# Optimization experiments

Hardware: AMD Instinct MI355X
Metric: run time of the kernel (lower is better)

## Reference

```python
import jax, jax.numpy as jnp
import numpy as np

EPS = 1e-06
NUM_HEADS = 8


def phi(x):
    # elu(x) + 1, a positive feature map
    return jax.nn.elu(x) + 1.0


def setup_inputs() -> dict:
    key = jax.random.key(0)
    ks = jax.random.split(key, 7)
    B, N, E = 4, 1024, 512
    s = 1.0 / np.sqrt(E)
    return {
        "Q": jax.random.normal(ks[0], (B, N, E), jnp.float32),
        "K": jax.random.normal(ks[1], (B, N, E), jnp.float32),
        "V": jax.random.normal(ks[2], (B, N, E), jnp.float32),
        "Wq": jax.random.normal(ks[3], (E, E), jnp.float32) * s,
        "Wk": jax.random.normal(ks[4], (E, E), jnp.float32) * s,
        "Wv": jax.random.normal(ks[5], (E, E), jnp.float32) * s,
        "Wo": jax.random.normal(ks[6], (E, E), jnp.float32) * s,
        "causal": 1,
    }


def _split_heads(x, H):
    B, N, E = x.shape
    return x.reshape(B, N, H, E // H).transpose(0, 2, 1, 3)  # (B,H,N,D)


def reference(Q, K, V, Wq, Wk, Wv, Wo, causal):
    B, N, E = Q.shape
    H = NUM_HEADS
    D = E // H
    # nn.Linear: y = x @ W.T (bias=False)
    Qf = phi(_split_heads(Q @ Wq.T, H))  # (B,H,N,D)
    Kf = phi(_split_heads(K @ Wk.T, H))  # (B,H,N,D)
    Vh = _split_heads(V @ Wv.T, H)       # (B,H,N,D)

    if causal:
        # prefix sums of outer products K_f V^T -> (B,H,N,D,Dv)
        KV_prefix = jnp.cumsum(Kf[..., :, None] * Vh[..., None, :], axis=2)
        Kf_prefix = jnp.cumsum(Kf, axis=2)
        num = jnp.einsum('bhnd,bhnde->bhne', Qf, KV_prefix)
        den = jnp.einsum('bhnd,bhnd->bhn', Qf, Kf_prefix)[..., None]
        out = num / (den + EPS)
    else:
        KV = jnp.einsum('bhnd,bhne->bhde', Kf, Vh)          # (B,H,D,Dv)
        Kf_sum = Kf.sum(axis=2)                              # (B,H,D)
        num = jnp.einsum('bhnd,bhde->bhne', Qf, KV)
        den = jnp.einsum('bhnd,bhd->bhn', Qf, Kf_sum)[..., None]
        out = num / (den + EPS)

    out = out.transpose(0, 2, 1, 3).reshape(B, N, E)
    return out @ Wo.T
```

## Files before the change

### kernel.cpp

```cpp
#include <hip/hip_runtime.h>
#include <stdint.h>

typedef __bf16 bf16;
typedef __attribute__((ext_vector_type(8))) __bf16 bfx8;
typedef __attribute__((ext_vector_type(4))) float f32x4;

__device__ inline f32x4 mfma16(bfx8 a, bfx8 b, f32x4 c) {
  return __builtin_amdgcn_mfma_f32_16x16x32_bf16(a, b, c, 0, 0, 0);
}

__device__ inline void gl16(const bf16* g, bf16* lbase, int lane) {
#if __has_builtin(__builtin_amdgcn_global_load_lds)
  (void)lane;
  __builtin_amdgcn_global_load_lds(
      (const __attribute__((address_space(1))) void*)g,
      (__attribute__((address_space(3))) void*)lbase, 16, 0, 0);
#else
  *(bfx8*)(lbase + lane * 8) = *(const bfx8*)g;
#endif
}

__device__ inline int img_off(int i, int e) {
  return i * 64 + ((((e >> 3) ^ (i & 7)) << 3)) + (e & 7);
}

struct CvtArgs {
  const float* src[4];
  bf16* dst[4];
};
__global__ __launch_bounds__(256) void cvt_w(CvtArgs ca) {
  const int z = blockIdx.y;
  const int T = blockIdx.x * 256 + threadIdx.x;
  const int n = T >> 3, s8 = T & 7, i = n & 63, nt = n >> 6;
  const float* src = ca.src[z];
  bf16* dst = ca.dst[z];
#pragma unroll
  for (int kt = 0; kt < 8; ++kt) {
    const float* s = src + (size_t)n * 512 + kt * 64 + ((s8 ^ (i & 7)) << 3);
    f32x4 x0 = *(const f32x4*)s, x1 = *(const f32x4*)(s + 4);
    bfx8 v;
    v[0] = (bf16)x0[0]; v[1] = (bf16)x0[1]; v[2] = (bf16)x0[2]; v[3] = (bf16)x0[3];
    v[4] = (bf16)x1[0]; v[5] = (bf16)x1[1]; v[6] = (bf16)x1[2]; v[7] = (bf16)x1[3];
    *(bfx8*)&dst[(size_t)(kt * 8 + nt) * 4096 + i * 64 + s8 * 8] = v;
  }
}

struct GemmArgs {
  const void* A[3];
  const bf16* Bt[3];
  bf16* ob[3];
  float* of;
  int phi_upto;
};

template <bool AF32, bool OUTF>
__global__ __launch_bounds__(256) void gemm_bt(GemmArgs ga) {
  const int z = blockIdx.z;
  const void* Ag = ga.A[z];
  const bf16* Bg = ga.Bt[z];
  const int tm = blockIdx.x * 64, by = blockIdx.y, tn = by * 128;
  const int tid = threadIdx.x, l = tid & 63, w = tid >> 6;
  const int wm = w >> 1, wn = w & 1, lm = l & 15, lk = l >> 4;

  __shared__ __align__(16) bf16 As[64 * 64];
  __shared__ __align__(16) bf16 Bs[128 * 64];

  f32x4 acc[2][4] = {};

  for (int kt = 0; kt < 8; ++kt) {
    const bf16* bsrc = Bg + (size_t)(kt * 8 + by * 2) * 4096;
#pragma unroll
    for (int q = 0; q < 4; ++q) {
      int cb = (q * 4 + w) * 64;
      gl16(bsrc + (size_t)(cb + l) * 8, &Bs[cb * 8], l);
    }
    if (AF32) {
#pragma unroll
      for (int it = 0; it < 2; ++it) {
        int c = it * 256 + tid;
        int row = c >> 3, t8 = c & 7;
        const float* s = (const float*)Ag + (size_t)(tm + row) * 512 + kt * 64 + t8 * 8;
        f32x4 x0 = *(const f32x4*)s, x1 = *(const f32x4*)(s + 4);
        bfx8 v;
        v[0] = (bf16)x0[0]; v[1] = (bf16)x0[1]; v[2] = (bf16)x0[2]; v[3] = (bf16)x0[3];
        v[4] = (bf16)x1[0]; v[5] = (bf16)x1[1]; v[6] = (bf16)x1[2]; v[7] = (bf16)x1[3];
        *(bfx8*)&As[row * 64 + ((t8 ^ (row & 7)) << 3)] = v;
      }
    } else {
      const bf16* asrc = (const bf16*)Ag + ((size_t)((tm >> 6) * 8 + kt) << 12);
#pragma unroll
      for (int q = 0; q < 2; ++q) {
        int cb = (q * 4 + w) * 64;
        gl16(asrc + (size_t)(cb + l) * 8, &As[cb * 8], l);
      }
    }
    __syncthreads();
#pragma unroll
    for (int ks = 0; ks < 2; ++ks) {
      bfx8 af[2], bfr[4];
#pragma unroll
      for (int i = 0; i < 2; ++i) {
        int ra = wm * 32 + i * 16 + lm;
        af[i] = *(const bfx8*)&As[ra * 64 + (((ks * 4 + lk) ^ (ra & 7)) << 3)];
      }
#pragma unroll
      for (int j = 0; j < 4; ++j) {
        int rb = wn * 64 + j * 16 + lm;
        bfr[j] = *(const bfx8*)&Bs[rb * 64 + (((ks * 4 + lk) ^ (rb & 7)) << 3)];
      }
#pragma unroll
      for (int i = 0; i < 2; ++i)
#pragma unroll
        for (int j = 0; j < 4; ++j)
          acc[i][j] = mfma16(af[i], bfr[j], acc[i][j]);
    }
    __syncthreads();
  }

  const bool phi = z < ga.phi_upto;
#pragma unroll
  for (int i = 0; i < 2; ++i)
#pragma unroll
    for (int j = 0; j < 4; ++j)
#pragma unroll
      for (int r = 0; r < 4; ++r) {
        int m = tm + wm * 32 + i * 16 + lk * 4 + r;
        int n = tn + wn * 64 + j * 16 + lm;
        float v = acc[i][j][r];
        if (phi) v = v > 0.f ? v + 1.f : __expf(v);
        if (OUTF) {
          ga.of[(size_t)m * 512 + n] = v;
        } else {
          ga.ob[z][((size_t)((m >> 6) * 8 + (n >> 6)) << 12) + img_off(m & 63, n & 63)] =
              (bf16)v;
        }
      }
}

__global__ __launch_bounds__(256) void chunk_kv(const bf16* __restrict__ Kimg,
                                                const bf16* __restrict__ Vimg,
                                                bf16* __restrict__ KVb,
                                                float* __restrict__ ksums) {
  const int bh = blockIdx.x, c = blockIdx.y, b = bh >> 3, h = bh & 7;
  const int tid = threadIdx.x, l = tid & 63, w = tid >> 6, lm = l & 15, lk = l >> 4;
  __shared__ __align__(16) bf16 KTs[64 * 64];
  __shared__ __align__(16) bf16 VTs[64 * 64];
  __shared__ float ksum_p[256];

  const size_t tb = (size_t)((b * 16 + c) * 8 + h) << 12;
  const bf16* Kt = Kimg + tb;
  const bf16* Vt = Vimg + tb;
  const int sr = tid >> 2, sp = tid & 3;
  {
    bfx8 k0 = *(const bfx8*)&Kt[sr * 64 + (((2 * sp) ^ (sr & 7)) << 3)];
    bfx8 k1 = *(const bfx8*)&Kt[sr * 64 + (((2 * sp + 1) ^ (sr & 7)) << 3)];
    bfx8 v0 = *(const bfx8*)&Vt[sr * 64 + (((2 * sp) ^ (sr & 7)) << 3)];
    bfx8 v1 = *(const bfx8*)&Vt[sr * 64 + (((2 * sp + 1) ^ (sr & 7)) << 3)];
#pragma unroll
    for (int q = 0; q < 8; ++q) {
      int d0 = sp * 16 + q, d1 = sp * 16 + 8 + q;
      KTs[d0 * 64 + (((sr >> 3) ^ (d0 & 7)) << 3) + (sr & 7)] = k0[q];
      KTs[d1 * 64 + (((sr >> 3) ^ (d1 & 7)) << 3) + (sr & 7)] = k1[q];
      VTs[d0 * 64 + (((sr >> 3) ^ (d0 & 7)) << 3) + (sr & 7)] = v0[q];
      VTs[d1 * 64 + (((sr >> 3) ^ (d1 & 7)) << 3) + (sr & 7)] = v1[q];
    }
  }
  __syncthreads();
  {
    int d = tid & 63, jp = tid >> 6;
    float s = 0.f;
#pragma unroll
    for (int q = 0; q < 16; ++q) {
      int j = jp * 16 + q;
      s += (float)KTs[d * 64 + (((j >> 3) ^ (d & 7)) << 3) + (j & 7)];
    }
    ksum_p[jp * 64 + d] = s;
  }
  f32x4 kacc[4] = {};
#pragma unroll
  for (int ks = 0; ks < 2; ++ks) {
    int r = w * 16 + lm;
    bfx8 av = *(const bfx8*)&VTs[r * 64 + (((ks * 4 + lk) ^ (r & 7)) << 3)];
#pragma unroll
    for (int bn = 0; bn < 4; ++bn) {
      int e = bn * 16 + lm;
      bfx8 bk = *(const bfx8*)&KTs[e * 64 + (((ks * 4 + lk) ^ (e & 7)) << 3)];
      kacc[bn] = mfma16(av, bk, kacc[bn]);
    }
  }
  bf16* st = KVb + (size_t)(bh * 16 + c) * 4096;
#pragma unroll
  for (int bn = 0; bn < 4; ++bn)
#pragma unroll
    for (int rg = 0; rg < 4; ++rg) {
      int e = w * 16 + lk * 4 + rg, d = bn * 16 + lm;
      st[e * 64 + d] = (bf16)kacc[bn][rg];
    }
  __syncthreads();
  if (tid < 64)
    ksums[(size_t)(bh * 16 + c) * 64 + tid] =
        ksum_p[tid] + ksum_p[64 + tid] + ksum_p[128 + tid] + ksum_p[192 + tid];
}

__global__ __launch_bounds__(256) void chunk_out(const bf16* __restrict__ Qimg,
                                                 const bf16* __restrict__ Kimg,
                                                 const bf16* __restrict__ Vimg,
                                                 const bf16* __restrict__ KVb,
                                                 const float* __restrict__ ksums,
                                                 bf16* __restrict__ Obsw) {
  const int bh = blockIdx.x, c = blockIdx.y, b = bh >> 3, h = bh & 7;
  const int tid = threadIdx.x, l = tid & 63, w = tid >> 6, lm = l & 15, lk = l >> 4;

  __shared__ __align__(16) bf16 Qs[64 * 64];
  __shared__ __align__(16) bf16 Ks[64 * 64];
  __shared__ __align__(16) bf16 VTs[64 * 64];
  __shared__ __align__(16) bf16 Ss[64 * 64];
  __shared__ __align__(16) bf16 KVL[64 * 64];
  __shared__ float ksum[64], den_i[64], den_all[64], den_p[256];

  const size_t tb = (size_t)((b * 16 + c) * 8 + h) << 12;
  const int sr = tid >> 2, sp = tid & 3;

#pragma unroll
  for (int q = 0; q < 2; ++q) {
    int cb = (q * 4 + w) * 64;
    gl16(Qimg + tb + (size_t)(cb + l) * 8, &Qs[cb * 8], l);
    gl16(Kimg + tb + (size_t)(cb + l) * 8, &Ks[cb * 8], l);
  }
  {
    const bf16* Vt = Vimg + tb;
    bfx8 v0 = *(const bfx8*)&Vt[sr * 64 + (((2 * sp) ^ (sr & 7)) << 3)];
    bfx8 v1 = *(const bfx8*)&Vt[sr * 64 + (((2 * sp + 1) ^ (sr & 7)) << 3)];
#pragma unroll
    for (int q = 0; q < 8; ++q) {
      int d0 = sp * 16 + q, d1 = sp * 16 + 8 + q;
      VTs[d0 * 64 + (((sr >> 3) ^ (d0 & 7)) << 3) + (sr & 7)] = v0[q];
      VTs[d1 * 64 + (((sr >> 3) ^ (d1 & 7)) << 3) + (sr & 7)] = v1[q];
    }
  }
  {
    const int e = sr, dp = sp * 16;
    float s0[8] = {}, s1[8] = {};
    const bf16* kb = KVb + (size_t)(bh * 16) * 4096 + e * 64 + dp;
    for (int cc = 0; cc < c; ++cc) {
      bfx8 x0 = *(const bfx8*)(kb + (size_t)cc * 4096);
      bfx8 x1 = *(const bfx8*)(kb + (size_t)cc * 4096 + 8);
#pragma unroll
      for (int q = 0; q < 8; ++q) { s0[q] += (float)x0[q]; s1[q] += (float)x1[q]; }
    }
    bfx8 y0, y1;
#pragma unroll
    for (int q = 0; q < 8; ++q) { y0[q] = (bf16)s0[q]; y1[q] = (bf16)s1[q]; }
    *(bfx8*)&KVL[e * 64 + (((2 * sp) ^ (e & 7)) << 3)] = y0;
    *(bfx8*)&KVL[e * 64 + (((2 * sp + 1) ^ (e & 7)) << 3)] = y1;
    if (tid < 64) {
      float s = 0.f;
      const float* kp = ksums + (size_t)(bh * 16) * 64 + tid;
      for (int cc = 0; cc < c; ++cc) s += kp[(size_t)cc * 64];
      ksum[tid] = s;
    }
  }
  __syncthreads();

  f32x4 sacc[4] = {};
  bfx8 aq[2];
#pragma unroll
  for (int ks = 0; ks < 2; ++ks) {
    int r = w * 16 + lm;
    aq[ks] = *(const bfx8*)&Qs[r * 64 + (((ks * 4 + lk) ^ (r & 7)) << 3)];
#pragma unroll
    for (int bn = 0; bn < 4; ++bn) {
// ... 31 lines not shown
    den_p[sp * 64 + sr] = s;
  }
  __syncthreads();

  if (tid < 64)
    den_all[tid] = den_i[tid] + den_p[tid] + den_p[64 + tid] + den_p[128 + tid] + den_p[192 + tid];
  f32x4 oacc[4] = {};
#pragma unroll
  for (int ks = 0; ks < 2; ++ks) {
    int r = w * 16 + lm;
    bfx8 as_ = *(const bfx8*)&Ss[r * 64 + (((ks * 4 + lk) ^ (r & 7)) << 3)];
#pragma unroll
    for (int bn = 0; bn < 4; ++bn) {
      int e = bn * 16 + lm;
      bfx8 bv = *(const bfx8*)&VTs[e * 64 + (((ks * 4 + lk) ^ (e & 7)) << 3)];
      oacc[bn] = mfma16(as_, bv, oacc[bn]);
      bfx8 bkv = *(const bfx8*)&KVL[e * 64 + (((ks * 4 + lk) ^ (e & 7)) << 3)];
      oacc[bn] = mfma16(aq[ks], bkv, oacc[bn]);
    }
  }
  __syncthreads();

  bf16* ot = Obsw + tb;
#pragma unroll
  for (int bn = 0; bn < 4; ++bn)
#pragma unroll
    for (int rg = 0; rg < 4; ++rg) {
      int i = w * 16 + lk * 4 + rg, e = bn * 16 + lm;
      float o = oacc[bn][rg] / (den_all[i] + 1e-6f);
      ot[img_off(i, e)] = (bf16)o;
    }
}

extern "C" void kernel_launch(void* const* d_in, const int* in_sizes, int n_in,
                              void* d_out, int out_size, void* d_ws, size_t ws_size,
                              hipStream_t stream) {
  const float* Q = (const float*)d_in[0];
  const float* K = (const float*)d_in[1];
  const float* V = (const float*)d_in[2];
  const float* Wq = (const float*)d_in[3];
  const float* Wk = (const float*)d_in[4];
  const float* Wv = (const float*)d_in[5];
  const float* Wo = (const float*)d_in[6];
  (void)in_sizes; (void)n_in; (void)out_size; (void)ws_size;

  char* wsp = (char*)d_ws;
  const size_t MB = 1ull << 20;
  const size_t HK = 512 * 1024;
  bf16* Wimg[4];
  for (int z = 0; z < 4; ++z) Wimg[z] = (bf16*)(wsp + z * HK);
  bf16* Qimg = (bf16*)(wsp + 4 * MB);
  bf16* Kimg = (bf16*)(wsp + 8 * MB);
  bf16* Vimg = (bf16*)(wsp + 12 * MB);
  bf16* Obsw = (bf16*)(wsp + 16 * MB);
  bf16* KVb = (bf16*)(wsp + 20 * MB);
  float* ksums = (float*)(wsp + 24 * MB);

  CvtArgs ca;
  ca.src[0] = Wq; ca.src[1] = Wk; ca.src[2] = Wv; ca.src[3] = Wo;
  ca.dst[0] = Wimg[0]; ca.dst[1] = Wimg[1]; ca.dst[2] = Wimg[2]; ca.dst[3] = Wimg[3];
  cvt_w<<<dim3(16, 4), 256, 0, stream>>>(ca);

  GemmArgs g1;
  g1.A[0] = Q;  g1.A[1] = K;  g1.A[2] = V;
  g1.Bt[0] = Wimg[0]; g1.Bt[1] = Wimg[1]; g1.Bt[2] = Wimg[2];
  g1.ob[0] = Qimg; g1.ob[1] = Kimg; g1.ob[2] = Vimg;
  g1.of = nullptr;
  g1.phi_upto = 2;
  gemm_bt<true, false><<<dim3(64, 4, 3), 256, 0, stream>>>(g1);

  chunk_kv<<<dim3(32, 16), 256, 0, stream>>>(Kimg, Vimg, KVb, ksums);
  chunk_out<<<dim3(32, 16), 256, 0, stream>>>(Qimg, Kimg, Vimg, KVb, ksums, Obsw);

  GemmArgs g2;
  g2.A[0] = Obsw; g2.A[1] = nullptr; g2.A[2] = nullptr;
  g2.Bt[0] = Wimg[3]; g2.Bt[1] = nullptr; g2.Bt[2] = nullptr;
  g2.ob[0] = nullptr; g2.ob[1] = nullptr; g2.ob[2] = nullptr;
  g2.of = (float*)d_out;
  g2.phi_upto = 0;
  gemm_bt<false, true><<<dim3(64, 4, 1), 256, 0, stream>>>(g2);
}
```

Baseline: 48.30 us.

## Double-buffer GEMM tiles and reuse transposed V image from chunk_kv in chunk_out

The GEMM kernel now double-buffers its A and B shared tiles, prefetching the next k-tile (DMA for B and bf16 A, register staging for fp32 A) while computing the current one, and drops one barrier per iteration. chunk_kv now loads K/V tiles into LDS via global_load_lds before transposing, and writes the transposed V tile to a new workspace image. chunk_out then DMA-loads that pre-transposed V instead of redoing the scalar LDS transpose. The cost is doubled GEMM LDS (lower occupancy), extra registers, and an extra global write and buffer for V^T.

```diff
diff --git a/kernel.cpp b/kernel.cpp
--- a/kernel.cpp
+++ b/kernel.cpp
@@ -62,51 +62,79 @@
   const int tid = threadIdx.x, l = tid & 63, w = tid >> 6;
   const int wm = w >> 1, wn = w & 1, lm = l & 15, lk = l >> 4;
 
-  __shared__ __align__(16) bf16 As[64 * 64];
-  __shared__ __align__(16) bf16 Bs[128 * 64];
+  __shared__ __align__(16) bf16 As[2][64 * 64];
+  __shared__ __align__(16) bf16 Bs[2][128 * 64];
 
   f32x4 acc[2][4] = {};
-
-  for (int kt = 0; kt < 8; ++kt) {
+  f32x4 a_reg[2][2];
+
+  auto issueB = [&](int kt, int buf) {
     const bf16* bsrc = Bg + (size_t)(kt * 8 + by * 2) * 4096;
 #pragma unroll
     for (int q = 0; q < 4; ++q) {
       int cb = (q * 4 + w) * 64;
-      gl16(bsrc + (size_t)(cb + l) * 8, &Bs[cb * 8], l);
-    }
-    if (AF32) {
-#pragma unroll
-      for (int it = 0; it < 2; ++it) {
-        int c = it * 256 + tid;
-        int row = c >> 3, t8 = c & 7;
-        const float* s = (const float*)Ag + (size_t)(tm + row) * 512 + kt * 64 + t8 * 8;
-        f32x4 x0 = *(const f32x4*)s, x1 = *(const f32x4*)(s + 4);
-        bfx8 v;
-        v[0] = (bf16)x0[0]; v[1] = (bf16)x0[1]; v[2] = (bf16)x0[2]; v[3] = (bf16)x0[3];
-        v[4] = (bf16)x1[0]; v[5] = (bf16)x1[1]; v[6] = (bf16)x1[2]; v[7] = (bf16)x1[3];
-        *(bfx8*)&As[row * 64 + ((t8 ^ (row & 7)) << 3)] = v;
-      }
-    } else {
-      const bf16* asrc = (const bf16*)Ag + ((size_t)((tm >> 6) * 8 + kt) << 12);
-#pragma unroll
-      for (int q = 0; q < 2; ++q) {
-        int cb = (q * 4 + w) * 64;
-        gl16(asrc + (size_t)(cb + l) * 8, &As[cb * 8], l);
-      }
-    }
-    __syncthreads();
+      gl16(bsrc + (size_t)(cb + l) * 8, &Bs[buf][cb * 8], l);
+    }
+  };
+  auto issueA_dma = [&](int kt, int buf) {
+    const bf16* asrc = (const bf16*)Ag + ((size_t)((tm >> 6) * 8 + kt) << 12);
+#pragma unroll
+    for (int q = 0; q < 2; ++q) {
+      int cb = (q * 4 + w) * 64;
+      gl16(asrc + (size_t)(cb + l) * 8, &As[buf][cb * 8], l);
+    }
+  };
+  auto loadA = [&](int kt) {
+#pragma unroll
+    for (int it = 0; it < 2; ++it) {
+      int c = it * 256 + tid;
+      int row = c >> 3, t8 = c & 7;
+      const float* s = (const float*)Ag + (size_t)(tm + row) * 512 + kt * 64 + t8 * 8;
+      a_reg[it][0] = *(const f32x4*)s;
+      a_reg[it][1] = *(const f32x4*)(s + 4);
+    }
+  };
+  auto writeA = [&](int buf) {
+#pragma unroll
+    for (int it = 0; it < 2; ++it) {
+      int c = it * 256 + tid;
+      int row = c >> 3, t8 = c & 7;
+      bfx8 v;
+      f32x4 x0 = a_reg[it][0], x1 = a_reg[it][1];
+      v[0] = (bf16)x0[0]; v[1] = (bf16)x0[1]; v[2] = (bf16)x0[2]; v[3] = (bf16)x0[3];
+      v[4] = (bf16)x1[0]; v[5] = (bf16)x1[1]; v[6] = (bf16)x1[2]; v[7] = (bf16)x1[3];
+      *(bfx8*)&As[buf][row * 64 + ((t8 ^ (row & 7)) << 3)] = v;
+    }
+  };
+
+  issueB(0, 0);
+  if constexpr (AF32) {
+    loadA(0);
+    writeA(0);
+  } else {
+    issueA_dma(0, 0);
+  }
+  __syncthreads();
+
+  for (int kt = 0; kt < 8; ++kt) {
+    const int cur = kt & 1, nxt = cur ^ 1;
+    if (kt < 7) {
+      issueB(kt + 1, nxt);
+      if constexpr (AF32) loadA(kt + 1);
+      else issueA_dma(kt + 1, nxt);
+    }
 #pragma unroll
     for (int ks = 0; ks < 2; ++ks) {
       bfx8 af[2], bfr[4];
 #pragma unroll
       for (int i = 0; i < 2; ++i) {
         int ra = wm * 32 + i * 16 + lm;
-        af[i] = *(const bfx8*)&As[ra * 64 + (((ks * 4 + lk) ^ (ra & 7)) << 3)];
+        af[i] = *(const bfx8*)&As[cur][ra * 64 + (((ks * 4 + lk) ^ (ra & 7)) << 3)];
       }
 #pragma unroll
       for (int j = 0; j < 4; ++j) {
         int rb = wn * 64 + j * 16 + lm;
-        bfr[j] = *(const bfx8*)&Bs[rb * 64 + (((ks * 4 + lk) ^ (rb & 7)) << 3)];
+        bfr[j] = *(const bfx8*)&Bs[cur][rb * 64 + (((ks * 4 + lk) ^ (rb & 7)) << 3)];
       }
 #pragma unroll
       for (int i = 0; i < 2; ++i)
@@ -114,7 +142,10 @@
         for (int j = 0; j < 4; ++j)
           acc[i][j] = mfma16(af[i], bfr[j], acc[i][j]);
     }
-    __syncthreads();
+    if (kt < 7) {
+      if constexpr (AF32) writeA(nxt);
+      __syncthreads();
+    }
   }
 
   const bool phi = z < ga.phi_upto;
@@ -140,22 +171,32 @@
 __global__ __launch_bounds__(256) void chunk_kv(const bf16* __restrict__ Kimg,
                                                 const bf16* __restrict__ Vimg,
                                                 bf16* __restrict__ KVb,
-                                                float* __restrict__ ksums) {
+                                                float* __restrict__ ksums,
+                                                bf16* __restrict__ VTimg) {
   const int bh = blockIdx.x, c = blockIdx.y, b = bh >> 3, h = bh & 7;
   const int tid = threadIdx.x, l = tid & 63, w = tid >> 6, lm = l & 15, lk = l >> 4;
+  __shared__ __align__(16) bf16 Ks[64 * 64];
+  __shared__ __align__(16) bf16 Vs[64 * 64];
   __shared__ __align__(16) bf16 KTs[64 * 64];
   __shared__ __align__(16) bf16 VTs[64 * 64];
   __shared__ float ksum_p[256];
 
   const size_t tb = (size_t)((b * 16 + c) * 8 + h) << 12;
-  const bf16* Kt = Kimg + tb;
-  const bf16* Vt = Vimg + tb;
   const int sr = tid >> 2, sp = tid & 3;
+
+#pragma unroll
+  for (int q = 0; q < 2; ++q) {
+    int cb = (q * 4 + w) * 64;
+    gl16(Kimg + tb + (size_t)(cb + l) * 8, &Ks[cb * 8], l);
+    gl16(Vimg + tb + (size_t)(cb + l) * 8, &Vs[cb * 8], l);
+  }
+  __syncthreads();
+
   {
-    bfx8 k0 = *(const bfx8*)&Kt[sr * 64 + (((2 * sp) ^ (sr & 7)) << 3)];
-    bfx8 k1 = *(const bfx8*)&Kt[sr * 64 + (((2 * sp + 1) ^ (sr & 7)) << 3)];
-    bfx8 v0 = *(const bfx8*)&Vt[sr * 64 + (((2 * sp) ^ (sr & 7)) << 3)];
-    bfx8 v1 = *(const bfx8*)&Vt[sr * 64 + (((2 * sp + 1) ^ (sr & 7)) << 3)];
+    bfx8 k0 = *(const bfx8*)&Ks[sr * 64 + (((2 * sp) ^ (sr & 7)) << 3)];
+    bfx8 k1 = *(const bfx8*)&Ks[sr * 64 + (((2 * sp + 1) ^ (sr & 7)) << 3)];
+    bfx8 v0 = *(const bfx8*)&Vs[sr * 64 + (((2 * sp) ^ (sr & 7)) << 3)];
+    bfx8 v1 = *(const bfx8*)&Vs[sr * 64 + (((2 * sp + 1) ^ (sr & 7)) << 3)];
 #pragma unroll
     for (int q = 0; q < 8; ++q) {
       int d0 = sp * 16 + q, d1 = sp * 16 + 8 + q;
@@ -166,6 +207,7 @@
     }
   }
   __syncthreads();
+
   {
     int d = tid & 63, jp = tid >> 6;
     float s = 0.f;
@@ -175,6 +217,11 @@
       s += (float)KTs[d * 64 + (((j >> 3) ^ (d & 7)) << 3) + (j & 7)];
     }
     ksum_p[jp * 64 + d] = s;
+  }
+#pragma unroll
+  for (int q = 0; q < 2; ++q) {
+    int cid = q * 256 + tid;
+    *(bfx8*)&VTimg[tb + (size_t)cid * 8] = *(const bfx8*)&VTs[cid * 8];
   }
   f32x4 kacc[4] = {};
 #pragma unroll
@@ -204,7 +251,7 @@
 
 __global__ __launch_bounds__(256) void chunk_out(const bf16* __restrict__ Qimg,
                                                  const bf16* __restrict__ Kimg,
-                                                 const bf16* __restrict__ Vimg,
+                                                 const bf16* __restrict__ VTimg,
                                                  const bf16* __restrict__ KVb,
                                                  const float* __restrict__ ksums,
                                                  bf16* __restrict__ Obsw) {
@@ -226,17 +273,7 @@
     int cb = (q * 4 + w) * 64;
     gl16(Qimg + tb + (size_t)(cb + l) * 8, &Qs[cb * 8], l);
     gl16(Kimg + tb + (size_t)(cb + l) * 8, &Ks[cb * 8], l);
-  }
-  {
-    const bf16* Vt = Vimg + tb;
-    bfx8 v0 = *(const bfx8*)&Vt[sr * 64 + (((2 * sp) ^ (sr & 7)) << 3)];
-    bfx8 v1 = *(const bfx8*)&Vt[sr * 64 + (((2 * sp + 1) ^ (sr & 7)) << 3)];
-#pragma unroll
-    for (int q = 0; q < 8; ++q) {
-      int d0 = sp * 16 + q, d1 = sp * 16 + 8 + q;
-      VTs[d0 * 64 + (((sr >> 3) ^ (d0 & 7)) << 3) + (sr & 7)] = v0[q];
-      VTs[d1 * 64 + (((sr >> 3) ^ (d1 & 7)) << 3) + (sr & 7)] = v1[q];
-    }
+    gl16(VTimg + tb + (size_t)(cb + l) * 8, &VTs[cb * 8], l);
   }
   {
     const int e = sr, dp = sp * 16;
@@ -357,6 +394,7 @@
   bf16* Obsw = (bf16*)(wsp + 16 * MB);
   bf16* KVb = (bf16*)(wsp + 20 * MB);
   float* ksums = (float*)(wsp + 24 * MB);
+  bf16* VTimg = (bf16*)(wsp + 28 * MB);
 
   CvtArgs ca;
   ca.src[0] = Wq; ca.src[1] = Wk; ca.src[2] = Wv; ca.src[3] = Wo;
@@ -371,8 +409,8 @@
   g1.phi_upto = 2;
   gemm_bt<true, false><<<dim3(64, 4, 3), 256, 0, stream>>>(g1);
 
-  chunk_kv<<<dim3(32, 16), 256, 0, stream>>>(Kimg, Vimg, KVb, ksums);
-  chunk_out<<<dim3(32, 16), 256, 0, stream>>>(Qimg, Kimg, Vimg, KVb, ksums, Obsw);
+  chunk_kv<<<dim3(32, 16), 256, 0, stream>>>(Kimg, Vimg, KVb, ksums, VTimg);
+  chunk_out<<<dim3(32, 16), 256, 0, stream>>>(Qimg, Kimg, VTimg, KVb, ksums, Obsw);
 
   GemmArgs g2;
   g2.A[0] = Obsw; g2.A[1] = nullptr; g2.A[2] = nullptr;
```

After: 49.35 us. +2.2%, slower.

## Fuse weight conversion, QKV projections and chunk KV into fewer kernels

Applied to the files above, without the earlier changes.

Removes the separate weight-conversion kernel by converting fp32 weights to bf16 on the fly inside each GEMM's tile load. Merges the K and V projections with the per-chunk KV outer-product and key-sum computation in one block, keeping K and V tiles in shared memory instead of re-reading them from global memory. This cuts the launch count from five to three. In exchange every block reconverts weight tiles redundantly, and K/V blocks run two serial GEMMs, so those blocks carry much more work than the Q blocks and the load becomes unbalanced.

```diff
diff --git a/kernel.cpp b/kernel.cpp
--- a/kernel.cpp
+++ b/kernel.cpp
@@ -24,75 +24,110 @@
   return i * 64 + ((((e >> 3) ^ (i & 7)) << 3)) + (e & 7);
 }
 
-struct CvtArgs {
-  const float* src[4];
-  bf16* dst[4];
+__device__ inline bfx8 cvt8(const float* s) {
+  f32x4 x0 = *(const f32x4*)s, x1 = *(const f32x4*)(s + 4);
+  bfx8 v;
+  v[0] = (bf16)x0[0]; v[1] = (bf16)x0[1]; v[2] = (bf16)x0[2]; v[3] = (bf16)x0[3];
+  v[4] = (bf16)x1[0]; v[5] = (bf16)x1[1]; v[6] = (bf16)x1[2]; v[7] = (bf16)x1[3];
+  return v;
+}
+
+struct ProjArgs {
+  const float *Q, *K, *V, *Wq, *Wk, *Wv;
+  bf16 *Qimg, *Kimg, *Vimg, *KVb;
+  float* ksums;
 };
-__global__ __launch_bounds__(256) void cvt_w(CvtArgs ca) {
-  const int z = blockIdx.y;
-  const int T = blockIdx.x * 256 + threadIdx.x;
-  const int n = T >> 3, s8 = T & 7, i = n & 63, nt = n >> 6;
-  const float* src = ca.src[z];
-  bf16* dst = ca.dst[z];
-#pragma unroll
-  for (int kt = 0; kt < 8; ++kt) {
-    const float* s = src + (size_t)n * 512 + kt * 64 + ((s8 ^ (i & 7)) << 3);
-    f32x4 x0 = *(const f32x4*)s, x1 = *(const f32x4*)(s + 4);
-    bfx8 v;
-    v[0] = (bf16)x0[0]; v[1] = (bf16)x0[1]; v[2] = (bf16)x0[2]; v[3] = (bf16)x0[3];
-    v[4] = (bf16)x1[0]; v[5] = (bf16)x1[1]; v[6] = (bf16)x1[2]; v[7] = (bf16)x1[3];
-    *(bfx8*)&dst[(size_t)(kt * 8 + nt) * 4096 + i * 64 + s8 * 8] = v;
-  }
-}
-
-struct GemmArgs {
-  const void* A[3];
-  const bf16* Bt[3];
-  bf16* ob[3];
-  float* of;
-  int phi_upto;
-};
-
-template <bool AF32, bool OUTF>
-__global__ __launch_bounds__(256) void gemm_bt(GemmArgs ga) {
-  const int z = blockIdx.z;
-  const void* Ag = ga.A[z];
-  const bf16* Bg = ga.Bt[z];
-  const int tm = blockIdx.x * 64, by = blockIdx.y, tn = by * 128;
+
+__global__ __launch_bounds__(256) void proj_fused(ProjArgs pa) {
   const int tid = threadIdx.x, l = tid & 63, w = tid >> 6;
   const int wm = w >> 1, wn = w & 1, lm = l & 15, lk = l >> 4;
-
-  __shared__ __align__(16) bf16 As[64 * 64];
-  __shared__ __align__(16) bf16 Bs[128 * 64];
-
-  f32x4 acc[2][4] = {};
-
+  __shared__ __align__(16) char smem[41984];
+  bf16* As = (bf16*)smem;
+  bf16* Bs = (bf16*)(smem + 8192);
+
+  const int bid = blockIdx.x;
+  const int idx = bid >> 1;
+
+  if ((bid & 1) == 0) {
+    const int tm = (idx >> 2) * 64, tn = (idx & 3) * 128;
+    f32x4 acc[2][4] = {};
+    for (int kt = 0; kt < 8; ++kt) {
+#pragma unroll
+      for (int it = 0; it < 4; ++it) {
+        int c = it * 256 + tid, row = c >> 3, t8 = c & 7;
+        bfx8 v = cvt8(pa.Wq + (size_t)(tn + row) * 512 + kt * 64 + t8 * 8);
+        *(bfx8*)&Bs[row * 64 + ((t8 ^ (row & 7)) << 3)] = v;
+      }
+#pragma unroll
+      for (int it = 0; it < 2; ++it) {
+        int c = it * 256 + tid, row = c >> 3, t8 = c & 7;
+        bfx8 v = cvt8(pa.Q + (size_t)(tm + row) * 512 + kt * 64 + t8 * 8);
+        *(bfx8*)&As[row * 64 + ((t8 ^ (row & 7)) << 3)] = v;
+      }
+      __syncthreads();
+#pragma unroll
+      for (int ks = 0; ks < 2; ++ks) {
+        bfx8 af[2], bfr[4];
+#pragma unroll
+        for (int i = 0; i < 2; ++i) {
+          int ra = wm * 32 + i * 16 + lm;
+          af[i] = *(const bfx8*)&As[ra * 64 + (((ks * 4 + lk) ^ (ra & 7)) << 3)];
+        }
+#pragma unroll
+        for (int j = 0; j < 4; ++j) {
+          int rb = wn * 64 + j * 16 + lm;
+          bfr[j] = *(const bfx8*)&Bs[rb * 64 + (((ks * 4 + lk) ^ (rb & 7)) << 3)];
+        }
+#pragma unroll
+        for (int i = 0; i < 2; ++i)
+#pragma unroll
+          for (int j = 0; j < 4; ++j)
+            acc[i][j] = mfma16(af[i], bfr[j], acc[i][j]);
+      }
+      __syncthreads();
+    }
+#pragma unroll
+    for (int i = 0; i < 2; ++i)
+#pragma unroll
+      for (int j = 0; j < 4; ++j)
+#pragma unroll
+        for (int r = 0; r < 4; ++r) {
+          int m = tm + wm * 32 + i * 16 + lk * 4 + r;
+          int n = tn + wn * 64 + j * 16 + lm;
+          float v = acc[i][j][r];
+          v = v > 0.f ? v + 1.f : __expf(v);
+          pa.Qimg[((size_t)((m >> 6) * 8 + (n >> 6)) << 12) + img_off(m & 63, n & 63)] =
+              (bf16)v;
+        }
+    return;
+  }
+
+  const int rt = idx >> 2, ty = idx & 3;
+  const int tm = rt * 64, tn = ty * 128;
+  bf16* VT0 = (bf16*)smem;
+  bf16* VT1 = (bf16*)(smem + 8192);
+  bf16* KT0 = (bf16*)(smem + 24576);
+  bf16* KT1 = (bf16*)(smem + 32768);
+  float* ksum_p = (float*)(smem + 40960);
+
+  f32x4 acc[2][4];
+
+#pragma unroll
+  for (int i = 0; i < 2; ++i)
+#pragma unroll
+    for (int j = 0; j < 4; ++j) acc[i][j] = (f32x4){0.f, 0.f, 0.f, 0.f};
   for (int kt = 0; kt < 8; ++kt) {
-    const bf16* bsrc = Bg + (size_t)(kt * 8 + by * 2) * 4096;
-#pragma unroll
-    for (int q = 0; q < 4; ++q) {
-      int cb = (q * 4 + w) * 64;
-      gl16(bsrc + (size_t)(cb + l) * 8, &Bs[cb * 8], l);
-    }
-    if (AF32) {
-#pragma unroll
-      for (int it = 0; it < 2; ++it) {
-        int c = it * 256 + tid;
-        int row = c >> 3, t8 = c & 7;
-        const float* s = (const float*)Ag + (size_t)(tm + row) * 512 + kt * 64 + t8 * 8;
-        f32x4 x0 = *(const f32x4*)s, x1 = *(const f32x4*)(s + 4);
-        bfx8 v;
-        v[0] = (bf16)x0[0]; v[1] = (bf16)x0[1]; v[2] = (bf16)x0[2]; v[3] = (bf16)x0[3];
-        v[4] = (bf16)x1[0]; v[5] = (bf16)x1[1]; v[6] = (bf16)x1[2]; v[7] = (bf16)x1[3];
-        *(bfx8*)&As[row * 64 + ((t8 ^ (row & 7)) << 3)] = v;
-      }
-    } else {
-      const bf16* asrc = (const bf16*)Ag + ((size_t)((tm >> 6) * 8 + kt) << 12);
-#pragma unroll
-      for (int q = 0; q < 2; ++q) {
-        int cb = (q * 4 + w) * 64;
-        gl16(asrc + (size_t)(cb + l) * 8, &As[cb * 8], l);
-      }
+#pragma unroll
+    for (int it = 0; it < 4; ++it) {
+      int c = it * 256 + tid, row = c >> 3, t8 = c & 7;
+      bfx8 v = cvt8(pa.Wk + (size_t)(tn + row) * 512 + kt * 64 + t8 * 8);
+      *(bfx8*)&Bs[row * 64 + ((t8 ^ (row & 7)) << 3)] = v;
+    }
+#pragma unroll
+    for (int it = 0; it < 2; ++it) {
+      int c = it * 256 + tid, row = c >> 3, t8 = c & 7;
+      bfx8 v = cvt8(pa.K + (size_t)(tm + row) * 512 + kt * 64 + t8 * 8);
+      *(bfx8*)&As[row * 64 + ((t8 ^ (row & 7)) << 3)] = v;
     }
     __syncthreads();
 #pragma unroll
@@ -116,90 +151,123 @@
     }
     __syncthreads();
   }
-
-  const bool phi = z < ga.phi_upto;
+  {
+    bf16* KTl = wn ? KT1 : KT0;
+#pragma unroll
+    for (int i = 0; i < 2; ++i)
+#pragma unroll
+      for (int jj = 0; jj < 4; ++jj)
+#pragma unroll
+        for (int r = 0; r < 4; ++r) {
+          int ml = wm * 32 + i * 16 + lk * 4 + r;
+          int dl = jj * 16 + lm;
+          float v = acc[i][jj][r];
+          v = v > 0.f ? v + 1.f : __expf(v);
+          bf16 bv = (bf16)v;
+          KTl[dl * 64 + (((ml >> 3) ^ (dl & 7)) << 3) + (ml & 7)] = bv;
+          pa.Kimg[((size_t)(rt * 8 + 2 * ty + wn) << 12) + img_off(ml, dl)] = bv;
+        }
+  }
+  __syncthreads();
+
 #pragma unroll
   for (int i = 0; i < 2; ++i)
 #pragma unroll
-    for (int j = 0; j < 4; ++j)
-#pragma unroll
-      for (int r = 0; r < 4; ++r) {
-        int m = tm + wm * 32 + i * 16 + lk * 4 + r;
-        int n = tn + wn * 64 + j * 16 + lm;
-        float v = acc[i][j][r];
-        if (phi) v = v > 0.f ? v + 1.f : __expf(v);
-        if (OUTF) {
-          ga.of[(size_t)m * 512 + n] = v;
-        } else {
-          ga.ob[z][((size_t)((m >> 6) * 8 + (n >> 6)) << 12) + img_off(m & 63, n & 63)] =
-              (bf16)v;
+    for (int j = 0; j < 4; ++j) acc[i][j] = (f32x4){0.f, 0.f, 0.f, 0.f};
+  for (int kt = 0; kt < 8; ++kt) {
+#pragma unroll
+    for (int it = 0; it < 4; ++it) {
+      int c = it * 256 + tid, row = c >> 3, t8 = c & 7;
+      bfx8 v = cvt8(pa.Wv + (size_t)(tn + row) * 512 + kt * 64 + t8 * 8);
+      *(bfx8*)&Bs[row * 64 + ((t8 ^ (row & 7)) << 3)] = v;
+    }
+#pragma unroll
+    for (int it = 0; it < 2; ++it) {
+      int c = it * 256 + tid, row = c >> 3, t8 = c & 7;
+      bfx8 v = cvt8(pa.V + (size_t)(tm + row) * 512 + kt * 64 + t8 * 8);
+      *(bfx8*)&As[row * 64 + ((t8 ^ (row & 7)) << 3)] = v;
+    }
+    __syncthreads();
+#pragma unroll
+    for (int ks = 0; ks < 2; ++ks) {
+      bfx8 af[2], bfr[4];
+#pragma unroll
+      for (int i = 0; i < 2; ++i) {
+        int ra = wm * 32 + i * 16 + lm;
+        af[i] = *(const bfx8*)&As[ra * 64 + (((ks * 4 + lk) ^ (ra & 7)) << 3)];
+      }
+#pragma unroll
+      for (int j = 0; j < 4; ++j) {
+        int rb = wn * 64 + j * 16 + lm;
+        bfr[j] = *(const bfx8*)&Bs[rb * 64 + (((ks * 4 + lk) ^ (rb & 7)) << 3)];
+      }
+#pragma unroll
+      for (int i = 0; i < 2; ++i)
+#pragma unroll
+        for (int j = 0; j < 4; ++j)
+          acc[i][j] = mfma16(af[i], bfr[j], acc[i][j]);
+    }
+    __syncthreads();
+  }
+  {
+    bf16* VTl = wn ? VT1 : VT0;
+#pragma unroll
+    for (int i = 0; i < 2; ++i)
+#pragma unroll
+      for (int jj = 0; jj < 4; ++jj)
+#pragma unroll
+        for (int r = 0; r < 4; ++r) {
+          int ml = wm * 32 + i * 16 + lk * 4 + r;
+          int dl = jj * 16 + lm;
+          bf16 bv = (bf16)acc[i][jj][r];
+          VTl[dl * 64 + (((ml >> 3) ^ (dl & 7)) << 3) + (ml & 7)] = bv;
+          pa.Vimg[((size_t)(rt * 8 + 2 * ty + wn) << 12) + img_off(ml, dl)] = bv;
         }
-      }
-}
-
-__global__ __launch_bounds__(256) void chunk_kv(const bf16* __restrict__ Kimg,
-                                                const bf16* __restrict__ Vimg,
-                                                bf16* __restrict__ KVb,
-                                                float* __restrict__ ksums) {
-  const int bh = blockIdx.x, c = blockIdx.y, b = bh >> 3, h = bh & 7;
-  const int tid = threadIdx.x, l = tid & 63, w = tid >> 6, lm = l & 15, lk = l >> 4;
-  __shared__ __align__(16) bf16 KTs[64 * 64];
-  __shared__ __align__(16) bf16 VTs[64 * 64];
-  __shared__ float ksum_p[256];
-
-  const size_t tb = (size_t)((b * 16 + c) * 8 + h) << 12;
-  const bf16* Kt = Kimg + tb;
-  const bf16* Vt = Vimg + tb;
-  const int sr = tid >> 2, sp = tid & 3;
-  {
-    bfx8 k0 = *(const bfx8*)&Kt[sr * 64 + (((2 * sp) ^ (sr & 7)) << 3)];
-    bfx8 k1 = *(const bfx8*)&Kt[sr * 64 + (((2 * sp + 1) ^ (sr & 7)) << 3)];
-    bfx8 v0 = *(const bfx8*)&Vt[sr * 64 + (((2 * sp) ^ (sr & 7)) << 3)];
-    bfx8 v1 = *(const bfx8*)&Vt[sr * 64 + (((2 * sp + 1) ^ (sr & 7)) << 3)];
-#pragma unroll
-    for (int q = 0; q < 8; ++q) {
-      int d0 = sp * 16 + q, d1 = sp * 16 + 8 + q;
-      KTs[d0 * 64 + (((sr >> 3) ^ (d0 & 7)) << 3) + (sr & 7)] = k0[q];
-      KTs[d1 * 64 + (((sr >> 3) ^ (d1 & 7)) << 3) + (sr & 7)] = k1[q];
-      VTs[d0 * 64 + (((sr >> 3) ^ (d0 & 7)) << 3) + (sr & 7)] = v0[q];
-      VTs[d1 * 64 + (((sr >> 3) ^ (d1 & 7)) << 3) + (sr & 7)] = v1[q];
-    }
   }
   __syncthreads();
-  {
-    int d = tid & 63, jp = tid >> 6;
-    float s = 0.f;
-#pragma unroll
-    for (int q = 0; q < 16; ++q) {
-      int j = jp * 16 + q;
-      s += (float)KTs[d * 64 + (((j >> 3) ^ (d & 7)) << 3) + (j & 7)];
-    }
-    ksum_p[jp * 64 + d] = s;
-  }
-  f32x4 kacc[4] = {};
-#pragma unroll
-  for (int ks = 0; ks < 2; ++ks) {
-    int r = w * 16 + lm;
-    bfx8 av = *(const bfx8*)&VTs[r * 64 + (((ks * 4 + lk) ^ (r & 7)) << 3)];
-#pragma unroll
-    for (int bn = 0; bn < 4; ++bn) {
-      int e = bn * 16 + lm;
-      bfx8 bk = *(const bfx8*)&KTs[e * 64 + (((ks * 4 + lk) ^ (e & 7)) << 3)];
-      kacc[bn] = mfma16(av, bk, kacc[bn]);
-    }
-  }
-  bf16* st = KVb + (size_t)(bh * 16 + c) * 4096;
-#pragma unroll
-  for (int bn = 0; bn < 4; ++bn)
-#pragma unroll
-    for (int rg = 0; rg < 4; ++rg) {
-      int e = w * 16 + lk * 4 + rg, d = bn * 16 + lm;
-      st[e * 64 + d] = (bf16)kacc[bn][rg];
-    }
-  __syncthreads();
-  if (tid < 64)
-    ksums[(size_t)(bh * 16 + c) * 64 + tid] =
-        ksum_p[tid] + ksum_p[64 + tid] + ksum_p[128 + tid] + ksum_p[192 + tid];
+
+  const int b = rt >> 4, c = rt & 15;
+#pragma unroll
+  for (int hh = 0; hh < 2; ++hh) {
+    const bf16* KTl = hh ? KT1 : KT0;
+    const bf16* VTl = hh ? VT1 : VT0;
+    {
+      int d = tid & 63, jp = tid >> 6;
+      float s = 0.f;
+#pragma unroll
+      for (int q = 0; q < 16; ++q) {
+        int j = jp * 16 + q;
+        s += (float)KTl[d * 64 + (((j >> 3) ^ (d & 7)) << 3) + (j & 7)];
+      }
+      ksum_p[jp * 64 + d] = s;
+    }
+    f32x4 kacc[4] = {};
+#pragma unroll
+    for (int ks = 0; ks < 2; ++ks) {
+      int r = w * 16 + lm;
+      bfx8 av = *(const bfx8*)&VTl[r * 64 + (((ks * 4 + lk) ^ (r & 7)) << 3)];
+#pragma unroll
+      for (int bn = 0; bn < 4; ++bn) {
+        int e = bn * 16 + lm;
+        bfx8 bk = *(const bfx8*)&KTl[e * 64 + (((ks * 4 + lk) ^ (e & 7)) << 3)];
+        kacc[bn] = mfma16(av, bk, kacc[bn]);
+      }
+    }
+    const int bh = b * 8 + 2 * ty + hh;
+    bf16* st = pa.KVb + (size_t)(bh * 16 + c) * 4096;
+#pragma unroll
+    for (int bn = 0; bn < 4; ++bn)
+#pragma unroll
+      for (int rg = 0; rg < 4; ++rg) {
+        int e = w * 16 + lk * 4 + rg, d = bn * 16 + lm;
+        st[e * 64 + d] = (bf16)kacc[bn][rg];
+      }
+    __syncthreads();
+    if (tid < 64)
+      pa.ksums[(size_t)(bh * 16 + c) * 64 + tid] =
+          ksum_p[tid] + ksum_p[64 + tid] + ksum_p[128 + tid] + ksum_p[192 + tid];
+    __syncthreads();
+  }
 }
 
 __global__ __launch_bounds__(256) void chunk_out(const bf16* __restrict__ Qimg,
@@ -334,51 +402,88 @@
     }
 }
 
+__global__ __launch_bounds__(256) void out_gemm(const bf16* __restrict__ Obsw,
+                                                const float* __restrict__ Wo,
+                                                float* __restrict__ out) {
+  const int bid = blockIdx.x;
+  const int tm = (bid >> 2) * 64, tn = (bid & 3) * 128;
+  const int tid = threadIdx.x, l = tid & 63, w = tid >> 6;
+  const int wm = w >> 1, wn = w & 1, lm = l & 15, lk = l >> 4;
+
+  __shared__ __align__(16) bf16 As[64 * 64];
+  __shared__ __align__(16) bf16 Bs[128 * 64];
+  f32x4 acc[2][4] = {};
+
+  for (int kt = 0; kt < 8; ++kt) {
+#pragma unroll
+    for (int it = 0; it < 4; ++it) {
+      int c = it * 256 + tid, row = c >> 3, t8 = c & 7;
+      bfx8 v = cvt8(Wo + (size_t)(tn + row) * 512 + kt * 64 + t8 * 8);
+      *(bfx8*)&Bs[row * 64 + ((t8 ^ (row & 7)) << 3)] = v;
+    }
+    const bf16* asrc = Obsw + ((size_t)((tm >> 6) * 8 + kt) << 12);
+#pragma unroll
+    for (int it = 0; it < 2; ++it) {
+      int c = it * 256 + tid;
+      *(bfx8*)&As[c * 8] = *(const bfx8*)(asrc + (size_t)c * 8);
+    }
+    __syncthreads();
+#pragma unroll
+    for (int ks = 0; ks < 2; ++ks) {
+      bfx8 af[2], bfr[4];
+#pragma unroll
+      for (int i = 0; i < 2; ++i) {
+        int ra = wm * 32 + i * 16 + lm;
+        af[i] = *(const bfx8*)&As[ra * 64 + (((ks * 4 + lk) ^ (ra & 7)) << 3)];
+      }
+#pragma unroll
+      for (int j = 0; j < 4; ++j) {
+        int rb = wn * 64 + j * 16 + lm;
+        bfr[j] = *(const bfx8*)&Bs[rb * 64 + (((ks * 4 + lk) ^ (rb & 7)) << 3)];
+      }
+#pragma unroll
+      for (int i = 0; i < 2; ++i)
+#pragma unroll
+        for (int j = 0; j < 4; ++j)
+          acc[i][j] = mfma16(af[i], bfr[j], acc[i][j]);
+    }
+    __syncthreads();
+  }
+#pragma unroll
+  for (int i = 0; i < 2; ++i)
+#pragma unroll
+    for (int j = 0; j < 4; ++j)
+#pragma unroll
+      for (int r = 0; r < 4; ++r) {
+        int m = tm + wm * 32 + i * 16 + lk * 4 + r;
+        int n = tn + wn * 64 + j * 16 + lm;
+        out[(size_t)m * 512 + n] = acc[i][j][r];
+      }
+}
+
 extern "C" void kernel_launch(void* const* d_in, const int* in_sizes, int n_in,
                               void* d_out, int out_size, void* d_ws, size_t ws_size,
                               hipStream_t stream) {
-  const float* Q = (const float*)d_in[0];
-  const float* K = (const float*)d_in[1];
-  const float* V = (const float*)d_in[2];
-  const float* Wq = (const float*)d_in[3];
-  const float* Wk = (const float*)d_in[4];
-  const float* Wv = (const float*)d_in[5];
-  const float* Wo = (const float*)d_in[6];
   (void)in_sizes; (void)n_in; (void)out_size; (void)ws_size;
-
   char* wsp = (char*)d_ws;
   const size_t MB = 1ull << 20;
-  const size_t HK = 512 * 1024;
-  bf16* Wimg[4];
-  for (int z = 0; z < 4; ++z) Wimg[z] = (bf16*)(wsp + z * HK);
-  bf16* Qimg = (bf16*)(wsp + 4 * MB);
-  bf16* Kimg = (bf16*)(wsp + 8 * MB);
-  bf16* Vimg = (bf16*)(wsp + 12 * MB);
-  bf16* Obsw = (bf16*)(wsp + 16 * MB);
-  bf16* KVb = (bf16*)(wsp + 20 * MB);
-  float* ksums = (float*)(wsp + 24 * MB);
-
-  CvtArgs ca;
-  ca.src[0] = Wq; ca.src[1] = Wk; ca.src[2] = Wv; ca.src[3] = Wo;
-  ca.dst[0] = Wimg[0]; ca.dst[1] = Wimg[1]; ca.dst[2] = Wimg[2]; ca.dst[3] = Wimg[3];
-  cvt_w<<<dim3(16, 4), 256, 0, stream>>>(ca);
-
-  GemmArgs g1;
-  g1.A[0] = Q;  g1.A[1] = K;  g1.A[2] = V;
-  g1.Bt[0] = Wimg[0]; g1.Bt[1] = Wimg[1]; g1.Bt[2] = Wimg[2];
-  g1.ob[0] = Qimg; g1.ob[1] = Kimg; g1.ob[2] = Vimg;
-  g1.of = nullptr;
-  g1.phi_upto = 2;
-  gemm_bt<true, false><<<dim3(64, 4, 3), 256, 0, stream>>>(g1);
-
-  chunk_kv<<<dim3(32, 16), 256, 0, stream>>>(Kimg, Vimg, KVb, ksums);
-  chunk_out<<<dim3(32, 16), 256, 0, stream>>>(Qimg, Kimg, Vimg, KVb, ksums, Obsw);
-
-  GemmArgs g2;
-  g2.A[0] = Obsw; g2.A[1] = nullptr; g2.A[2] = nullptr;
-  g2.Bt[0] = Wimg[3]; g2.Bt[1] = nullptr; g2.Bt[2] = nullptr;
-  g2.ob[0] = nullptr; g2.ob[1] = nullptr; g2.ob[2] = nullptr;
-  g2.of = (float*)d_out;
-  g2.phi_upto = 0;
-  gemm_bt<false, true><<<dim3(64, 4, 1), 256, 0, stream>>>(g2);
-}
+
+  ProjArgs pa;
+  pa.Q = (const float*)d_in[0];
+  pa.K = (const float*)d_in[1];
+  pa.V = (const float*)d_in[2];
+  pa.Wq = (const float*)d_in[3];
+  pa.Wk = (const float*)d_in[4];
+  pa.Wv = (const float*)d_in[5];
+  pa.Qimg = (bf16*)(wsp + 0 * MB);
+  pa.Kimg = (bf16*)(wsp + 4 * MB);
+  pa.Vimg = (bf16*)(wsp + 8 * MB);
+  pa.KVb = (bf16*)(wsp + 16 * MB);
+  pa.ksums = (float*)(wsp + 20 * MB);
+  bf16* Obsw = (bf16*)(wsp + 12 * MB);
+
+  proj_fused<<<512, 256, 0, stream>>>(pa);
+  chunk_out<<<dim3(32, 16), 256, 0, stream>>>(pa.Qimg, pa.Kimg, pa.Vimg, pa.KVb,
+                                              pa.ksums, Obsw);
+  out_gemm<<<256, 256, 0, stream>>>(Obsw, (const float*)d_in[6], (float*)d_out);
+}
```

After: 57.56 us. 19.2% more time.

## Fuse weight fp32-to-bf16 conversion into projection GEMMs and drop cvt kernel

Applied to the files above, without the earlier changes.

Removes the separate weight conversion kernel: both the QKV projection GEMM and the new output GEMM now read fp32 weights and convert them to bf16 while staging tiles into shared memory. This saves one launch and a bf16 weight image round trip, but each block repeats the weight conversion and uses plain vector loads instead of global_load_lds. The chunk_out grid is also reordered so the largest causal chunks (highest c) are scheduled first, aiming at better tail balance.

```diff
diff --git a/kernel.cpp b/kernel.cpp
--- a/kernel.cpp
+++ b/kernel.cpp
@@ -24,75 +24,45 @@
   return i * 64 + ((((e >> 3) ^ (i & 7)) << 3)) + (e & 7);
 }
 
-struct CvtArgs {
-  const float* src[4];
-  bf16* dst[4];
+__device__ inline bfx8 cvt8(const float* s) {
+  f32x4 x0 = *(const f32x4*)s, x1 = *(const f32x4*)(s + 4);
+  bfx8 v;
+  v[0] = (bf16)x0[0]; v[1] = (bf16)x0[1]; v[2] = (bf16)x0[2]; v[3] = (bf16)x0[3];
+  v[4] = (bf16)x1[0]; v[5] = (bf16)x1[1]; v[6] = (bf16)x1[2]; v[7] = (bf16)x1[3];
+  return v;
+}
+
+struct P3Args {
+  const float *Q, *K, *V, *Wq, *Wk, *Wv;
+  bf16 *Qimg, *Kimg, *Vimg;
 };
-__global__ __launch_bounds__(256) void cvt_w(CvtArgs ca) {
-  const int z = blockIdx.y;
-  const int T = blockIdx.x * 256 + threadIdx.x;
-  const int n = T >> 3, s8 = T & 7, i = n & 63, nt = n >> 6;
-  const float* src = ca.src[z];
-  bf16* dst = ca.dst[z];
-#pragma unroll
-  for (int kt = 0; kt < 8; ++kt) {
-    const float* s = src + (size_t)n * 512 + kt * 64 + ((s8 ^ (i & 7)) << 3);
-    f32x4 x0 = *(const f32x4*)s, x1 = *(const f32x4*)(s + 4);
-    bfx8 v;
-    v[0] = (bf16)x0[0]; v[1] = (bf16)x0[1]; v[2] = (bf16)x0[2]; v[3] = (bf16)x0[3];
-    v[4] = (bf16)x1[0]; v[5] = (bf16)x1[1]; v[6] = (bf16)x1[2]; v[7] = (bf16)x1[3];
-    *(bfx8*)&dst[(size_t)(kt * 8 + nt) * 4096 + i * 64 + s8 * 8] = v;
-  }
-}
-
-struct GemmArgs {
-  const void* A[3];
-  const bf16* Bt[3];
-  bf16* ob[3];
-  float* of;
-  int phi_upto;
-};
-
-template <bool AF32, bool OUTF>
-__global__ __launch_bounds__(256) void gemm_bt(GemmArgs ga) {
+
+__global__ __launch_bounds__(256) void proj3(P3Args pa) {
   const int z = blockIdx.z;
-  const void* Ag = ga.A[z];
-  const bf16* Bg = ga.Bt[z];
-  const int tm = blockIdx.x * 64, by = blockIdx.y, tn = by * 128;
+  const float* Ag = (z == 0) ? pa.Q : (z == 1) ? pa.K : pa.V;
+  const float* Wg = (z == 0) ? pa.Wq : (z == 1) ? pa.Wk : pa.Wv;
+  bf16* ob = (z == 0) ? pa.Qimg : (z == 1) ? pa.Kimg : pa.Vimg;
+  const bool phi = z < 2;
+  const int tm = blockIdx.x * 64, tn = blockIdx.y * 128;
   const int tid = threadIdx.x, l = tid & 63, w = tid >> 6;
   const int wm = w >> 1, wn = w & 1, lm = l & 15, lk = l >> 4;
 
   __shared__ __align__(16) bf16 As[64 * 64];
   __shared__ __align__(16) bf16 Bs[128 * 64];
-
   f32x4 acc[2][4] = {};
 
   for (int kt = 0; kt < 8; ++kt) {
-    const bf16* bsrc = Bg + (size_t)(kt * 8 + by * 2) * 4096;
-#pragma unroll
-    for (int q = 0; q < 4; ++q) {
-      int cb = (q * 4 + w) * 64;
-      gl16(bsrc + (size_t)(cb + l) * 8, &Bs[cb * 8], l);
-    }
-    if (AF32) {
-#pragma unroll
-      for (int it = 0; it < 2; ++it) {
-        int c = it * 256 + tid;
-        int row = c >> 3, t8 = c & 7;
-        const float* s = (const float*)Ag + (size_t)(tm + row) * 512 + kt * 64 + t8 * 8;
-        f32x4 x0 = *(const f32x4*)s, x1 = *(const f32x4*)(s + 4);
-        bfx8 v;
-        v[0] = (bf16)x0[0]; v[1] = (bf16)x0[1]; v[2] = (bf16)x0[2]; v[3] = (bf16)x0[3];
-        v[4] = (bf16)x1[0]; v[5] = (bf16)x1[1]; v[6] = (bf16)x1[2]; v[7] = (bf16)x1[3];
-        *(bfx8*)&As[row * 64 + ((t8 ^ (row & 7)) << 3)] = v;
-      }
-    } else {
-      const bf16* asrc = (const bf16*)Ag + ((size_t)((tm >> 6) * 8 + kt) << 12);
-#pragma unroll
-      for (int q = 0; q < 2; ++q) {
-        int cb = (q * 4 + w) * 64;
-        gl16(asrc + (size_t)(cb + l) * 8, &As[cb * 8], l);
-      }
+#pragma unroll
+    for (int it = 0; it < 4; ++it) {
+      int c = it * 256 + tid, row = c >> 3, t8 = c & 7;
+      bfx8 v = cvt8(Wg + (size_t)(tn + row) * 512 + kt * 64 + t8 * 8);
+      *(bfx8*)&Bs[row * 64 + ((t8 ^ (row & 7)) << 3)] = v;
+    }
+#pragma unroll
+    for (int it = 0; it < 2; ++it) {
+      int c = it * 256 + tid, row = c >> 3, t8 = c & 7;
+      bfx8 v = cvt8(Ag + (size_t)(tm + row) * 512 + kt * 64 + t8 * 8);
+      *(bfx8*)&As[row * 64 + ((t8 ^ (row & 7)) << 3)] = v;
     }
     __syncthreads();
 #pragma unroll
@@ -117,7 +87,6 @@
     __syncthreads();
   }
 
-  const bool phi = z < ga.phi_upto;
 #pragma unroll
   for (int i = 0; i < 2; ++i)
 #pragma unroll
@@ -128,12 +97,8 @@
         int n = tn + wn * 64 + j * 16 + lm;
         float v = acc[i][j][r];
         if (phi) v = v > 0.f ? v + 1.f : __expf(v);
-        if (OUTF) {
-          ga.of[(size_t)m * 512 + n] = v;
-        } else {
-          ga.ob[z][((size_t)((m >> 6) * 8 + (n >> 6)) << 12) + img_off(m & 63, n & 63)] =
-              (bf16)v;
-        }
+        ob[((size_t)((m >> 6) * 8 + (n >> 6)) << 12) + img_off(m & 63, n & 63)] =
+            (bf16)v;
       }
 }
 
@@ -208,7 +173,7 @@
                                                  const bf16* __restrict__ KVb,
                                                  const float* __restrict__ ksums,
                                                  bf16* __restrict__ Obsw) {
-  const int bh = blockIdx.x, c = blockIdx.y, b = bh >> 3, h = bh & 7;
+  const int c = 15 - blockIdx.x, bh = blockIdx.y, b = bh >> 3, h = bh & 7;
   const int tid = threadIdx.x, l = tid & 63, w = tid >> 6, lm = l & 15, lk = l >> 4;
 
   __shared__ __align__(16) bf16 Qs[64 * 64];
@@ -334,51 +299,89 @@
     }
 }
 
+__global__ __launch_bounds__(256) void out_gemm(const bf16* __restrict__ Obsw,
+                                                const float* __restrict__ Wo,
+                                                float* __restrict__ out) {
+  const int bid = blockIdx.x;
+  const int tm = (bid >> 2) * 64, tn = (bid & 3) * 128;
+  const int tid = threadIdx.x, l = tid & 63, w = tid >> 6;
+  const int wm = w >> 1, wn = w & 1, lm = l & 15, lk = l >> 4;
+
+  __shared__ __align__(16) bf16 As[64 * 64];
+  __shared__ __align__(16) bf16 Bs[128 * 64];
+  f32x4 acc[2][4] = {};
+
+  for (int kt = 0; kt < 8; ++kt) {
+#pragma unroll
+    for (int it = 0; it < 4; ++it) {
+      int c = it * 256 + tid, row = c >> 3, t8 = c & 7;
+      bfx8 v = cvt8(Wo + (size_t)(tn + row) * 512 + kt * 64 + t8 * 8);
+      *(bfx8*)&Bs[row * 64 + ((t8 ^ (row & 7)) << 3)] = v;
+    }
+    const bf16* asrc = Obsw + ((size_t)((tm >> 6) * 8 + kt) << 12);
+#pragma unroll
+    for (int it = 0; it < 2; ++it) {
+      int c = it * 256 + tid;
+      *(bfx8*)&As[c * 8] = *(const bfx8*)(asrc + (size_t)c * 8);
+    }
+    __syncthreads();
+#pragma unroll
+    for (int ks = 0; ks < 2; ++ks) {
+      bfx8 af[2], bfr[4];
+#pragma unroll
+      for (int i = 0; i < 2; ++i) {
+        int ra = wm * 32 + i * 16 + lm;
+        af[i] = *(const bfx8*)&As[ra * 64 + (((ks * 4 + lk) ^ (ra & 7)) << 3)];
+      }
+#pragma unroll
+      for (int j = 0; j < 4; ++j) {
+        int rb = wn * 64 + j * 16 + lm;
+        bfr[j] = *(const bfx8*)&Bs[rb * 64 + (((ks * 4 + lk) ^ (rb & 7)) << 3)];
+      }
+#pragma unroll
+      for (int i = 0; i < 2; ++i)
+#pragma unroll
+        for (int j = 0; j < 4; ++j)
+          acc[i][j] = mfma16(af[i], bfr[j], acc[i][j]);
+    }
+    __syncthreads();
+  }
+#pragma unroll
+  for (int i = 0; i < 2; ++i)
+#pragma unroll
+    for (int j = 0; j < 4; ++j)
+#pragma unroll
+      for (int r = 0; r < 4; ++r) {
+        int m = tm + wm * 32 + i * 16 + lk * 4 + r;
+        int n = tn + wn * 64 + j * 16 + lm;
+        out[(size_t)m * 512 + n] = acc[i][j][r];
+      }
+}
+
 extern "C" void kernel_launch(void* const* d_in, const int* in_sizes, int n_in,
                               void* d_out, int out_size, void* d_ws, size_t ws_size,
                               hipStream_t stream) {
-  const float* Q = (const float*)d_in[0];
-  const float* K = (const float*)d_in[1];
-  const float* V = (const float*)d_in[2];
-  const float* Wq = (const float*)d_in[3];
-  const float* Wk = (const float*)d_in[4];
-  const float* Wv = (const float*)d_in[5];
-  const float* Wo = (const float*)d_in[6];
   (void)in_sizes; (void)n_in; (void)out_size; (void)ws_size;
-
   char* wsp = (char*)d_ws;
   const size_t MB = 1ull << 20;
-  const size_t HK = 512 * 1024;
-  bf16* Wimg[4];
-  for (int z = 0; z < 4; ++z) Wimg[z] = (bf16*)(wsp + z * HK);
-  bf16* Qimg = (bf16*)(wsp + 4 * MB);
-  bf16* Kimg = (bf16*)(wsp + 8 * MB);
-  bf16* Vimg = (bf16*)(wsp + 12 * MB);
-  bf16* Obsw = (bf16*)(wsp + 16 * MB);
-  bf16* KVb = (bf16*)(wsp + 20 * MB);
-  float* ksums = (float*)(wsp + 24 * MB);
-
-  CvtArgs ca;
-  ca.src[0] = Wq; ca.src[1] = Wk; ca.src[2] = Wv; ca.src[3] = Wo;
-  ca.dst[0] = Wimg[0]; ca.dst[1] = Wimg[1]; ca.dst[2] = Wimg[2]; ca.dst[3] = Wimg[3];
-  cvt_w<<<dim3(16, 4), 256, 0, stream>>>(ca);
-
-  GemmArgs g1;
-  g1.A[0] = Q;  g1.A[1] = K;  g1.A[2] = V;
-  g1.Bt[0] = Wimg[0]; g1.Bt[1] = Wimg[1]; g1.Bt[2] = Wimg[2];
-  g1.ob[0] = Qimg; g1.ob[1] = Kimg; g1.ob[2] = Vimg;
-  g1.of = nullptr;
-  g1.phi_upto = 2;
-  gemm_bt<true, false><<<dim3(64, 4, 3), 256, 0, stream>>>(g1);
-
-  chunk_kv<<<dim3(32, 16), 256, 0, stream>>>(Kimg, Vimg, KVb, ksums);
-  chunk_out<<<dim3(32, 16), 256, 0, stream>>>(Qimg, Kimg, Vimg, KVb, ksums, Obsw);
-
-  GemmArgs g2;
-  g2.A[0] = Obsw; g2.A[1] = nullptr; g2.A[2] = nullptr;
-  g2.Bt[0] = Wimg[3]; g2.Bt[1] = nullptr; g2.Bt[2] = nullptr;
-  g2.ob[0] = nullptr; g2.ob[1] = nullptr; g2.ob[2] = nullptr;
-  g2.of = (float*)d_out;
-  g2.phi_upto = 0;
-  gemm_bt<false, true><<<dim3(64, 4, 1), 256, 0, stream>>>(g2);
-}
+
+  P3Args pa;
+  pa.Q = (const float*)d_in[0];
+  pa.K = (const float*)d_in[1];
+  pa.V = (const float*)d_in[2];
+  pa.Wq = (const float*)d_in[3];
+  pa.Wk = (const float*)d_in[4];
+  pa.Wv = (const float*)d_in[5];
+  pa.Qimg = (bf16*)(wsp + 0 * MB);
+  pa.Kimg = (bf16*)(wsp + 4 * MB);
+  pa.Vimg = (bf16*)(wsp + 8 * MB);
+  bf16* Obsw = (bf16*)(wsp + 12 * MB);
+  bf16* KVb = (bf16*)(wsp + 16 * MB);
+  float* ksums = (float*)(wsp + 20 * MB);
+
+  proj3<<<dim3(64, 4, 3), 256, 0, stream>>>(pa);
+  chunk_kv<<<dim3(32, 16), 256, 0, stream>>>(pa.Kimg, pa.Vimg, KVb, ksums);
+  chunk_out<<<dim3(16, 32), 256, 0, stream>>>(pa.Qimg, pa.Kimg, pa.Vimg, KVb,
+                                              ksums, Obsw);
+  out_gemm<<<256, 256, 0, stream>>>(Obsw, (const float*)d_in[6], (float*)d_out);
+}
```

Result: slower. 59.66 us (+23.5%).
